# Performance work log

Measured on AMD Instinct MI355X. Metric: run time of the kernel, lower is better.

Reference implementation:

```python
import jax, jax.numpy as jnp
import numpy as np

L, DIM, S = 4, 17, 4
B, H, W = 4, 256, 256
BINSIZE = 16.0


def setup_inputs() -> dict:
    key = jax.random.key(0)
    k1, k2, k3, k4 = jax.random.split(key, 4)
    lut = jax.random.normal(k1, (L, DIM, DIM, DIM, DIM, S, S), dtype=jnp.float32)
    tri_index = jax.random.normal(k2, (24, 4), dtype=jnp.float32)
    weight = jax.random.uniform(k3, (B, L, H, W), dtype=jnp.float32)
    x = jax.random.uniform(k4, (B, 1, H, W), dtype=jnp.float32) * 255.0
    return {"lut": lut, "tri_index": tri_index, "weight": weight, "x": x, "scale_factor": S}


def _quadrilinear(lut, weight, x, s):
    # lut: [L, D, D, D, D, s, s]; weight: [B, L, H, W]; x: [B, 1, H, W] in [0,255]
    Bx, C, Hx, Wx = x.shape
    Lx, D = lut.shape[0], lut.shape[1]
    # reflection pad right/bottom by 1, take the 2x2 neighborhood -> 4 LUT coords
    xp = jnp.pad(x, ((0, 0), (0, 0), (0, 1), (0, 1)), mode="reflect")
    pix = jnp.stack([xp[:, :, :Hx, :Wx], xp[:, :, :Hx, 1:Wx + 1],
                     xp[:, :, 1:Hx + 1, :Wx], xp[:, :, 1:Hx + 1, 1:Wx + 1]], axis=-1)  # [B,C,H,W,4]
    t = pix / BINSIZE
    base_f = jnp.floor(t)
    frac = t - base_f                                   # [B,C,H,W,4] in [0,1)
    base = jnp.clip(base_f, 0, D - 2).astype(jnp.int32)  # [B,C,H,W,4]
    # 4D simplex (generalized tetrahedral) interpolation: sort fracs descending
    order = jnp.argsort(-frac, axis=-1)                 # [B,C,H,W,4]
    sf = jnp.take_along_axis(frac, order, axis=-1)      # sorted desc
    wts = jnp.stack([1.0 - sf[..., 0],
                     sf[..., 0] - sf[..., 1],
                     sf[..., 1] - sf[..., 2],
                     sf[..., 2] - sf[..., 3],
                     sf[..., 3]], axis=-1)              # [B,C,H,W,5]
    oneh = jax.nn.one_hot(order, 4, dtype=jnp.int32)    # [B,C,H,W,4,4]
    cum = jnp.cumsum(oneh, axis=-2)                     # vertex k offset = sum of top-k one-hots
    offs = jnp.concatenate([jnp.zeros_like(cum[..., :1, :]), cum], axis=-2)  # [B,C,H,W,5,4]
    vidx = base[..., None, :] + offs                    # [B,C,H,W,5,4]
    flat = ((vidx[..., 0] * D + vidx[..., 1]) * D + vidx[..., 2]) * D + vidx[..., 3]  # [B,C,H,W,5]
    lut_flat = lut.reshape(Lx, D ** 4, s * s)
    gathered = lut_flat[:, flat]                        # [L,B,C,H,W,5,s*s]
    interp = jnp.einsum("lbchwks,bchwk->lbchws", gathered, wts)  # [L,B,C,H,W,s*s]
    out = jnp.einsum("lbchws,blhw->bchws", interp, weight)       # [B,C,H,W,s*s]
    out = out.reshape(Bx, C, Hx, Wx, s, s).transpose(0, 1, 2, 4, 3, 5)
    return out.reshape(Bx, C, Hx * s, Wx * s)


def reference(lut, tri_index, weight, x, scale_factor):
    # tri_index encodes the precomputed simplex permutation table used by the CUDA
    # kernel; the reference derives the permutation analytically (argsort), so it is unused.
    return _quadrilinear(lut, weight, x, int(scale_factor))
```

## Files before the change

### kernel.cpp

```cpp
#include <hip/hip_runtime.h>
#include <hip/hip_fp16.h>

#define HH   256
#define WW   256
#define HWPX (HH * WW)
#define DD   17
#define D4   (17 * 17 * 17 * 17)
#define NL   4
#define SS   16
#define LUT_FLOATS  (NL * D4 * SS)
#define LUT_BYTES_H ((size_t)LUT_FLOATS * 2)

__global__ __launch_bounds__(256) void lut_transpose_h_kernel(
    const float4* __restrict__ src,
    ushort* __restrict__ dst)
{
    int t = blockIdx.x * blockDim.x + threadIdx.x;
    if (t >= D4 * NL * 4) return;
    int c4 = t & 3;
    int l  = (t >> 2) & 3;
    int v  = t >> 4;
    float4 r = src[(size_t)l * (D4 * 4) + (size_t)v * 4 + c4];
    ushort4 h;
    h.x = __half_as_ushort(__float2half_rn(r.x));
    h.y = __half_as_ushort(__float2half_rn(r.y));
    h.z = __half_as_ushort(__float2half_rn(r.z));
    h.w = __half_as_ushort(__float2half_rn(r.w));
    *((ushort4*)(dst + (size_t)t * 4)) = h;
}

__global__ __launch_bounds__(256) void lut4d_kernel_qh(
    const ushort* __restrict__ lutT,
    const float* __restrict__ weight,
    const float* __restrict__ x,
    float* __restrict__ out)
{
    int tid = blockIdx.x * blockDim.x + threadIdx.x;
    int j = tid & 3;
    int p = tid >> 2;
    int b  = p >> 16;
    int hw = p & 65535;
    int h  = hw >> 8;
    int w  = hw & 255;

    const float* xb = x + b * HWPX;
    int h1 = (h + 1 < HH) ? (h + 1) : (HH - 2);
    int w1 = (w + 1 < WW) ? (w + 1) : (WW - 2);

    float pix0 = xb[h  * WW + w ];
    float pix1 = xb[h  * WW + w1];
    float pix2 = xb[h1 * WW + w ];
    float pix3 = xb[h1 * WW + w1];

    const float inv = 1.0f / 16.0f;
    float t0 = pix0 * inv, t1 = pix1 * inv, t2 = pix2 * inv, t3 = pix3 * inv;
    float bf0 = floorf(t0), bf1 = floorf(t1), bf2 = floorf(t2), bf3 = floorf(t3);
    float f0 = t0 - bf0, f1 = t1 - bf1, f2 = t2 - bf2, f3 = t3 - bf3;

    int b0 = min(max((int)bf0, 0), DD - 2);
    int b1 = min(max((int)bf1, 0), DD - 2);
    int b2 = min(max((int)bf2, 0), DD - 2);
    int b3 = min(max((int)bf3, 0), DD - 2);

    float s0f = f0, s1f = f1, s2f = f2, s3f = f3;
    int   s0s = 4913, s1s = 289, s2s = 17, s3s = 1;

#define CSWAP(fa, sa, fb, sb)                                          \
    do {                                                               \
        bool sw = (fb > fa) || ((fb == fa) && (sb > sa));              \
        float tf = fa; int ts = sa;                                    \
        if (sw) { fa = fb; sa = sb; fb = tf; sb = ts; }                \
    } while (0)

    CSWAP(s0f, s0s, s1f, s1s);
    CSWAP(s2f, s2s, s3f, s3s);
    CSWAP(s0f, s0s, s2f, s2s);
    CSWAP(s1f, s1s, s3f, s3s);
    CSWAP(s1f, s1s, s2f, s2s);
#undef CSWAP

    float wts[5];
    wts[0] = 1.0f - s0f;
    wts[1] = s0f - s1f;
    wts[2] = s1f - s2f;
    wts[3] = s2f - s3f;
    wts[4] = s3f;

    int flats[5];
    flats[0] = ((b0 * DD + b1) * DD + b2) * DD + b3;
    flats[1] = flats[0] + s0s;
    flats[2] = flats[1] + s1s;
    flats[3] = flats[2] + s2s;
    flats[4] = flats[3] + s3s;

    const float* wb = weight + b * (NL * HWPX) + hw;
    float wl[NL];
#pragma unroll
    for (int l = 0; l < NL; ++l) wl[l] = wb[l * HWPX];

    uint2 r[5][NL];
#pragma unroll
    for (int k = 0; k < 5; ++k) {
        const ushort* vbase = lutT + (size_t)flats[k] * (NL * SS);
#pragma unroll
        for (int l = 0; l < NL; ++l) {
            r[k][l] = *((const uint2*)(vbase + l * SS + j * 4));
        }
    }

    float a0 = 0.f, a1 = 0.f, a2 = 0.f, a3 = 0.f;
#pragma unroll
    for (int k = 0; k < 5; ++k) {
#pragma unroll
        for (int l = 0; l < NL; ++l) {
            float c = wl[l] * wts[k];
            __half2 h01 = *reinterpret_cast<const __half2*>(&r[k][l].x);
            __half2 h23 = *reinterpret_cast<const __half2*>(&r[k][l].y);
            float2 f01 = __half22float2(h01);
            float2 f23 = __half22float2(h23);
            a0 = fmaf(c, f01.x, a0);
            a1 = fmaf(c, f01.y, a1);
            a2 = fmaf(c, f23.x, a2);
            a3 = fmaf(c, f23.y, a3);
        }
    }

    float* ob = out + (size_t)b * (HH * 4) * (WW * 4)
                    + (size_t)(h * 4 + j) * (WW * 4) + (w * 4);
    *((float4*)ob) = make_float4(a0, a1, a2, a3);
}

__global__ __launch_bounds__(256) void lut4d_kernel_fallback(
    const float* __restrict__ lut,
    const float* __restrict__ weight,
    const float* __restrict__ x,
    float* __restrict__ out)
{
    int p = blockIdx.x * blockDim.x + threadIdx.x;
    int b  = p >> 16;
    int hw = p & 65535;
    int h  = hw >> 8;
    int w  = hw & 255;

    const float* xb = x + b * HWPX;
    int h1 = (h + 1 < HH) ? (h + 1) : (HH - 2);
    int w1 = (w + 1 < WW) ? (w + 1) : (WW - 2);

    float pix0 = xb[h  * WW + w ];
    float pix1 = xb[h  * WW + w1];
    float pix2 = xb[h1 * WW + w ];
    float pix3 = xb[h1 * WW + w1];

    const float inv = 1.0f / 16.0f;
    float t0 = pix0 * inv, t1 = pix1 * inv, t2 = pix2 * inv, t3 = pix3 * inv;
    float bf0 = floorf(t0), bf1 = floorf(t1), bf2 = floorf(t2), bf3 = floorf(t3);
    float f0 = t0 - bf0, f1 = t1 - bf1, f2 = t2 - bf2, f3 = t3 - bf3;

    int b0 = min(max((int)bf0, 0), DD - 2);
    int b1 = min(max((int)bf1, 0), DD - 2);
    int b2 = min(max((int)bf2, 0), DD - 2);
    int b3 = min(max((int)bf3, 0), DD - 2);

    float s0f = f0, s1f = f1, s2f = f2, s3f = f3;
    int   s0s = 4913, s1s = 289, s2s = 17, s3s = 1;

#define CSWAP(fa, sa, fb, sb)                                          \
    do {                                                               \
        bool sw = (fb > fa) || ((fb == fa) && (sb > sa));              \
        float tf = fa; int ts = sa;                                    \
        if (sw) { fa = fb; sa = sb; fb = tf; sb = ts; }                \
    } while (0)

    CSWAP(s0f, s0s, s1f, s1s);
    CSWAP(s2f, s2s, s3f, s3s);
    CSWAP(s0f, s0s, s2f, s2s);
    CSWAP(s1f, s1s, s3f, s3s);
    CSWAP(s1f, s1s, s2f, s2s);
#undef CSWAP

    float wts[5] = { 1.0f - s0f, s0f - s1f, s1f - s2f, s2f - s3f, s3f };
    int flats[5];
    flats[0] = ((b0 * DD + b1) * DD + b2) * DD + b3;
    flats[1] = flats[0] + s0s;
    flats[2] = flats[1] + s1s;
    flats[3] = flats[2] + s2s;
    flats[4] = flats[3] + s3s;

    float acc[SS];
#pragma unroll
    for (int i = 0; i < SS; ++i) acc[i] = 0.0f;

    const float* wb = weight + b * (NL * HWPX) + hw;

#pragma unroll
    for (int l = 0; l < NL; ++l) {
        float wlv = wb[l * HWPX];
        const float* lbase = lut + (size_t)l * D4 * SS;
#pragma unroll
        for (int k = 0; k < 5; ++k) {
            float c = wlv * wts[k];
            const float4* row = (const float4*)(lbase + (size_t)flats[k] * SS);
#pragma unroll
            for (int q = 0; q < 4; ++q) {
                float4 rr = row[q];
                acc[q * 4 + 0] = fmaf(c, rr.x, acc[q * 4 + 0]);
                acc[q * 4 + 1] = fmaf(c, rr.y, acc[q * 4 + 1]);
                acc[q * 4 + 2] = fmaf(c, rr.z, acc[q * 4 + 2]);
                acc[q * 4 + 3] = fmaf(c, rr.w, acc[q * 4 + 3]);
            }
        }
    }

    float* ob = out + (size_t)b * (HH * 4) * (WW * 4) + (size_t)(h * 4) * (WW * 4) + (w * 4);
#pragma unroll
    for (int i = 0; i < 4; ++i) {
        *((float4*)(ob + (size_t)i * (WW * 4))) =
            make_float4(acc[i * 4 + 0], acc[i * 4 + 1], acc[i * 4 + 2], acc[i * 4 + 3]);
    }
}

extern "C" void kernel_launch(void* const* d_in, const int* in_sizes, int n_in,
                              void* d_out, int out_size, void* d_ws, size_t ws_size,
                              hipStream_t stream) {
    const float* lut    = (const float*)d_in[0];
    const float* weight = (const float*)d_in[2];
    const float* x      = (const float*)d_in[3];
    float* out          = (float*)d_out;

    dim3 block(256);

    if (ws_size >= LUT_BYTES_H) {
        ushort* lutT = (ushort*)d_ws;
        int n_chunks = D4 * NL * 4;
        dim3 grid_t((n_chunks + 255) / 256);
        hipLaunchKernelGGL(lut_transpose_h_kernel, grid_t, block, 0, stream,
                           (const float4*)lut, lutT);
        dim3 grid_main(4096);
        hipLaunchKernelGGL(lut4d_kernel_qh, grid_main, block, 0, stream,
                           lutT, weight, x, out);
    } else {
        dim3 grid_main(1024);
        hipLaunchKernelGGL(lut4d_kernel_fallback, grid_main, block, 0, stream,
                           lut, weight, x, out);
    }
}
```

Baseline: 99.66 us.

## Split each pixel across 16 lanes covering layer and output row, reduce via shuffles

The main kernel now gives each pixel 16 threads instead of 4, with each thread handling one LUT layer and one output row. Each thread issues a single contiguous 8-byte load per simplex vertex, and the four layer partial sums are combined with xor shuffles before one lane per row writes. This raises memory-level parallelism and makes each vertex's 128-byte record read contiguously across lanes. The cost is four times more threads, each redundantly repeating the pixel load, sort and index math, plus the shuffle reduction and idle lanes during the store.

```diff
diff --git a/kernel.cpp b/kernel.cpp
--- a/kernel.cpp
+++ b/kernel.cpp
@@ -29,15 +29,17 @@
     *((ushort4*)(dst + (size_t)t * 4)) = h;
 }
 
-__global__ __launch_bounds__(256) void lut4d_kernel_qh(
+__global__ __launch_bounds__(256) void lut4d_kernel_c16(
     const ushort* __restrict__ lutT,
     const float* __restrict__ weight,
     const float* __restrict__ x,
     float* __restrict__ out)
 {
     int tid = blockIdx.x * blockDim.x + threadIdx.x;
-    int j = tid & 3;
-    int p = tid >> 2;
+    int j     = tid & 15;
+    int l_idx = j >> 2;
+    int q     = j & 3;
+    int p = tid >> 4;
     int b  = p >> 16;
     int hw = p & 65535;
     int h  = hw >> 8;
@@ -93,41 +95,39 @@
     flats[3] = flats[2] + s2s;
     flats[4] = flats[3] + s3s;
 
-    const float* wb = weight + b * (NL * HWPX) + hw;
-    float wl[NL];
-#pragma unroll
-    for (int l = 0; l < NL; ++l) wl[l] = wb[l * HWPX];
-
-    uint2 r[5][NL];
+    float wl = weight[(size_t)b * (NL * HWPX) + (size_t)l_idx * HWPX + hw];
+
+    uint2 r[5];
 #pragma unroll
     for (int k = 0; k < 5; ++k) {
         const ushort* vbase = lutT + (size_t)flats[k] * (NL * SS);
-#pragma unroll
-        for (int l = 0; l < NL; ++l) {
-            r[k][l] = *((const uint2*)(vbase + l * SS + j * 4));
-        }
+        r[k] = *((const uint2*)(vbase + j * 4));
     }
 
     float a0 = 0.f, a1 = 0.f, a2 = 0.f, a3 = 0.f;
 #pragma unroll
     for (int k = 0; k < 5; ++k) {
-#pragma unroll
-        for (int l = 0; l < NL; ++l) {
-            float c = wl[l] * wts[k];
-            __half2 h01 = *reinterpret_cast<const __half2*>(&r[k][l].x);
-            __half2 h23 = *reinterpret_cast<const __half2*>(&r[k][l].y);
-            float2 f01 = __half22float2(h01);
-            float2 f23 = __half22float2(h23);
-            a0 = fmaf(c, f01.x, a0);
-            a1 = fmaf(c, f01.y, a1);
-            a2 = fmaf(c, f23.x, a2);
-            a3 = fmaf(c, f23.y, a3);
-        }
-    }
-
-    float* ob = out + (size_t)b * (HH * 4) * (WW * 4)
-                    + (size_t)(h * 4 + j) * (WW * 4) + (w * 4);
-    *((float4*)ob) = make_float4(a0, a1, a2, a3);
+        float c = wl * wts[k];
+        __half2 h01 = *reinterpret_cast<const __half2*>(&r[k].x);
+        __half2 h23 = *reinterpret_cast<const __half2*>(&r[k].y);
+        float2 f01 = __half22float2(h01);
+        float2 f23 = __half22float2(h23);
+        a0 = fmaf(c, f01.x, a0);
+        a1 = fmaf(c, f01.y, a1);
+        a2 = fmaf(c, f23.x, a2);
+        a3 = fmaf(c, f23.y, a3);
+    }
+
+    a0 += __shfl_xor(a0, 4);  a0 += __shfl_xor(a0, 8);
+    a1 += __shfl_xor(a1, 4);  a1 += __shfl_xor(a1, 8);
+    a2 += __shfl_xor(a2, 4);  a2 += __shfl_xor(a2, 8);
+    a3 += __shfl_xor(a3, 4);  a3 += __shfl_xor(a3, 8);
+
+    if (l_idx == 0) {
+        float* ob = out + (size_t)b * (HH * 4) * (WW * 4)
+                        + (size_t)(h * 4 + q) * (WW * 4) + (w * 4);
+        *((float4*)ob) = make_float4(a0, a1, a2, a3);
+    }
 }
 
 __global__ __launch_bounds__(256) void lut4d_kernel_fallback(
@@ -201,12 +201,12 @@
             float c = wlv * wts[k];
             const float4* row = (const float4*)(lbase + (size_t)flats[k] * SS);
 #pragma unroll
-            for (int q = 0; q < 4; ++q) {
-                float4 rr = row[q];
-                acc[q * 4 + 0] = fmaf(c, rr.x, acc[q * 4 + 0]);
-                acc[q * 4 + 1] = fmaf(c, rr.y, acc[q * 4 + 1]);
-                acc[q * 4 + 2] = fmaf(c, rr.z, acc[q * 4 + 2]);
-                acc[q * 4 + 3] = fmaf(c, rr.w, acc[q * 4 + 3]);
+            for (int qq = 0; qq < 4; ++qq) {
+                float4 rr = row[qq];
+                acc[qq * 4 + 0] = fmaf(c, rr.x, acc[qq * 4 + 0]);
+                acc[qq * 4 + 1] = fmaf(c, rr.y, acc[qq * 4 + 1]);
+                acc[qq * 4 + 2] = fmaf(c, rr.z, acc[qq * 4 + 2]);
+                acc[qq * 4 + 3] = fmaf(c, rr.w, acc[qq * 4 + 3]);
             }
         }
     }
@@ -235,8 +235,8 @@
         dim3 grid_t((n_chunks + 255) / 256);
         hipLaunchKernelGGL(lut_transpose_h_kernel, grid_t, block, 0, stream,
                            (const float4*)lut, lutT);
-        dim3 grid_main(4096);
-        hipLaunchKernelGGL(lut4d_kernel_qh, grid_main, block, 0, stream,
+        dim3 grid_main(16384);
+        hipLaunchKernelGGL(lut4d_kernel_c16, grid_main, block, 0, stream,
                            lutT, weight, x, out);
     } else {
         dim3 grid_main(1024);
```

New measurement: 101.7 us. +2.1%, slower.
